# Performance work log

Hardware: AMD Instinct MI355X
Metric: run time of the kernel (lower is better)

The kernel has to match this reference:

```python
import jax, jax.numpy as jnp
import numpy as np

N = 100000      # nodes
E = 1600000     # edges (before self-loops)
F_IN = 128      # dataset.num_node_features
H, C = 8, 8     # heads, hid
D = H * C       # 64, concat output dim
G = 64          # graphs in batch
N_CLS = 10
SLOPE = 0.2     # PyG GATConv negative_slope default


def setup_inputs() -> dict:
    key = jax.random.key(0)
    ks = jax.random.split(key, 16)
    s = 0.1
    return {
        "x": jax.random.normal(ks[0], (N, F_IN), jnp.float32),
        "edge_index": jax.random.randint(ks[1], (2, E), 0, N, jnp.int32),
        "batch": jnp.sort(jax.random.randint(ks[2], (N,), 0, G, jnp.int32)),
        "W1": jax.random.normal(ks[3], (F_IN, D), jnp.float32) * s,
        "a1_src": jax.random.normal(ks[4], (H, C), jnp.float32) * s,
        "a1_dst": jax.random.normal(ks[5], (H, C), jnp.float32) * s,
        "b1": jnp.zeros((D,), jnp.float32),
        "W2": jax.random.normal(ks[6], (D, D), jnp.float32) * s,
        "a2_src": jax.random.normal(ks[7], (H, C), jnp.float32) * s,
        "a2_dst": jax.random.normal(ks[8], (H, C), jnp.float32) * s,
        "b2": jnp.zeros((D,), jnp.float32),
        "W3": jax.random.normal(ks[9], (D, D), jnp.float32) * s,
        "a3_src": jax.random.normal(ks[10], (H, C), jnp.float32) * s,
        "a3_dst": jax.random.normal(ks[11], (H, C), jnp.float32) * s,
        "b3": jnp.zeros((D,), jnp.float32),
        "lin_W": jax.random.normal(ks[12], (D, N_CLS), jnp.float32) * s,
        "lin_b": jnp.zeros((N_CLS,), jnp.float32),
    }


def _gat_conv(h_in, src, dst, W, a_src, a_dst, b):
    # h: [N, H, C] per-head projected features
    h = (h_in @ W).reshape(N, H, C)
    al_src = jnp.einsum('nhc,hc->nh', h, a_src)  # [N, H]
    al_dst = jnp.einsum('nhc,hc->nh', h, a_dst)
    e = al_src[src] + al_dst[dst]                # [E', H]
    e = jnp.where(e > 0, e, SLOPE * e)           # LeakyReLU
    # segment softmax over incoming edges of each dst node
    m = jax.ops.segment_max(e, dst, num_segments=N)          # every node has a self-loop
    e = jnp.exp(e - m[dst])
    denom = jax.ops.segment_sum(e, dst, num_segments=N)
    alpha = e / denom[dst]                        # [E', H]
    out = jax.ops.segment_sum(h[src] * alpha[:, :, None], dst, num_segments=N)
    return out.reshape(N, D) + b


def reference(x, edge_index, batch, W1, a1_src, a1_dst, b1,
              W2, a2_src, a2_dst, b2, W3, a3_src, a3_dst, b3, lin_W, lin_b):
    # PyG GATConv add_self_loops=True
    loop = jnp.arange(N, dtype=edge_index.dtype)
    src = jnp.concatenate([edge_index[0], loop])
    dst = jnp.concatenate([edge_index[1], loop])

    h = jax.nn.elu(_gat_conv(x, src, dst, W1, a1_src, a1_dst, b1))
    h = jax.nn.elu(_gat_conv(h, src, dst, W2, a2_src, a2_dst, b2))
    h = jax.nn.elu(_gat_conv(h, src, dst, W3, a3_src, a3_dst, b3))

    # global mean pool over graph assignment
    sums = jax.ops.segment_sum(h, batch, num_segments=G)          # [G, D]
    cnts = jax.ops.segment_sum(jnp.ones((N,), h.dtype), batch, num_segments=G)
    pooled = sums / jnp.maximum(cnts, 1.0)[:, None]

    return pooled @ lin_W + lin_b  # [G, N_CLS]
```

## Files before the change

### kernel.cpp

```cpp
#include <hip/hip_runtime.h>
#include <math.h>

#define NN 100000
#define EE 1600000
#define GG 64
#define NCLS 10

#define BSH 8
#define NB 391
#define BCAP 4608
#define EPS 4096
#define CAPS 5120

typedef unsigned int uint32;

__device__ __forceinline__ unsigned short f2bf(float f) {
    unsigned u = __float_as_uint(f);
    unsigned r = (u + 0x7fffu + ((u >> 16) & 1u)) >> 16;
    return (unsigned short)r;
}


__global__ __launch_bounds__(512) void bscatter_kernel(
    const int* __restrict__ src, const int* __restrict__ dst,
    int* __restrict__ bfill, uint32* __restrict__ bpack, int n) {
    __shared__ int hist[512], gbase[512], lbase[512], cnt2[512];
    __shared__ int wtot[8];
    __shared__ uint32 lsd[EPS];
    __shared__ unsigned short bkt[EPS];
    int tid = threadIdx.x;
    int lane = tid & 63, wv = tid >> 6;
    int e0 = blockIdx.x * EPS;
    int e1 = min(e0 + EPS, n);

    hist[tid] = 0;
    cnt2[tid] = 0;
    __syncthreads();
    for (int e = e0 + tid; e < e1; e += 512) atomicAdd(&hist[dst[e] >> BSH], 1);
    __syncthreads();
    int h = hist[tid];
    int inc = h;
#pragma unroll
    for (int off = 1; off < 64; off <<= 1) {
        int t = __shfl_up(inc, off);
        if (lane >= off) inc += t;
    }
    if (lane == 63) wtot[wv] = inc;
    __syncthreads();
    if (tid < 8) {
        int t = wtot[tid];
#pragma unroll
        for (int off = 1; off < 8; off <<= 1) {
            int u = __shfl_up(t, off, 8);
            if (tid >= off) t += u;
        }
        wtot[tid] = t;
    }
    __syncthreads();
    if (wv > 0) inc += wtot[wv - 1];
    int lb = inc - h;
    lbase[tid] = lb;
    int go = h > 0 ? atomicAdd(&bfill[tid], h) : 0;
    gbase[tid] = tid * BCAP + go - lb;
    __syncthreads();
    for (int e = e0 + tid; e < e1; e += 512) {
        int s = src[e], dd = dst[e];
        int b = dd >> BSH;
        int r = atomicAdd(&cnt2[b], 1);
        int slot = lbase[b] + r;
        lsd[slot] = ((uint32)s << 8) | (uint32)(dd & 255);
        bkt[slot] = (unsigned short)b;
    }
    __syncthreads();
    int m = e1 - e0;
    for (int i = tid; i < m; i += 512)
        bpack[gbase[bkt[i]] + i] = lsd[i];
}

__global__ __launch_bounds__(256) void bsort_kernel(
    const uint32* __restrict__ bpack, const int* __restrict__ bfill,
    int* __restrict__ rp, int* __restrict__ re, int* __restrict__ col) {
    __shared__ int cnt[256], cnt2[256];
    __shared__ int wtot[4];
    __shared__ int stage[CAPS];
    int b = blockIdx.x;
    int tid = threadIdx.x;
    int ebeg = b * BCAP;
    int sz = bfill[b];
    int n0 = b << BSH;
    int nn = min(256, NN - n0);

    cnt[tid] = 0;
    cnt2[tid] = 0;
    __syncthreads();
    const uint4* bq = (const uint4*)(bpack + ebeg);
    int nq = sz >> 2;
    for (int i = tid; i < nq; i += 256) {
        uint4 p = bq[i];
        atomicAdd(&cnt[p.x & 255u], 1);
        atomicAdd(&cnt[p.y & 255u], 1);
        atomicAdd(&cnt[p.z & 255u], 1);
        atomicAdd(&cnt[p.w & 255u], 1);
    }
    for (int e = (nq << 2) + tid; e < sz; e += 256)
        atomicAdd(&cnt[bpack[ebeg + e] & 255u], 1);
    __syncthreads();
    int lane = tid & 63, wv = tid >> 6;
    int c = cnt[tid];
    int inc = c;
#pragma unroll
    for (int off = 1; off < 64; off <<= 1) {
        int t = __shfl_up(inc, off);
        if (lane >= off) inc += t;
    }
    if (lane == 63) wtot[wv] = inc;
    __syncthreads();
    if (tid < 4) {
        int t = wtot[tid];
#pragma unroll
        for (int off = 1; off < 4; off <<= 1) {
            int u = __shfl_up(t, off, 4);
            if (tid >= off) t += u;
        }
        wtot[tid] = t;
    }
    __syncthreads();
    if (wv > 0) inc += wtot[wv - 1];
    int excl = inc - c;
    cnt[tid] = excl;
    if (tid < nn) {
        rp[n0 + tid] = ebeg + excl;
        re[n0 + tid] = ebeg + inc;
    }
    __syncthreads();
    bool fits = sz <= CAPS;
    for (int i = tid; i < nq; i += 256) {
        uint4 p = bq[i];
        int d0 = (int)(p.x & 255u), d1 = (int)(p.y & 255u);
        int d2 = (int)(p.z & 255u), d3 = (int)(p.w & 255u);
        int p0 = cnt[d0] + atomicAdd(&cnt2[d0], 1);
        int p1 = cnt[d1] + atomicAdd(&cnt2[d1], 1);
        int p2 = cnt[d2] + atomicAdd(&cnt2[d2], 1);
        int p3 = cnt[d3] + atomicAdd(&cnt2[d3], 1);
        if (fits) {
            stage[p0] = (int)(p.x >> 8); stage[p1] = (int)(p.y >> 8);
            stage[p2] = (int)(p.z >> 8); stage[p3] = (int)(p.w >> 8);
        } else {
            col[ebeg + p0] = (int)(p.x >> 8); col[ebeg + p1] = (int)(p.y >> 8);
            col[ebeg + p2] = (int)(p.z >> 8); col[ebeg + p3] = (int)(p.w >> 8);
        }
    }
    for (int e = (nq << 2) + tid; e < sz; e += 256) {
        uint32 p = bpack[ebeg + e];
        int dl = (int)(p & 255u);
        int pos = cnt[dl] + atomicAdd(&cnt2[dl], 1);
        if (fits) stage[pos] = (int)(p >> 8);
        else col[ebeg + pos] = (int)(p >> 8);
    }
    __syncthreads();
    if (fits) {
        uint4* colq = (uint4*)(col + ebeg);
        const uint4* stq = (const uint4*)stage;
        for (int i = tid; i < nq; i += 256) colq[i] = stq[i];
        for (int i = (nq << 2) + tid; i < sz; i += 256) col[ebeg + i] = stage[i];
    }
}


template <int K>
__global__ __launch_bounds__(256) void gemm_al_kernel(
    const float* __restrict__ X, const float* __restrict__ W,
    const float* __restrict__ a_src, const float* __restrict__ a_dst,
    unsigned short* __restrict__ H, float* __restrict__ ALs, float* __restrict__ ALd,
    int nrows) {
    const int KC = 64;
    const int KP = KC + 4;
    __shared__ float Xs[64 * (KC + 4)];
    __shared__ float Ws[K * 64];
    int tid = threadIdx.x;
    int r0 = blockIdx.x * 64;
    int validRows = min(64, nrows - r0);

    {
        const float4* Wg = (const float4*)W;
        float4* Ws4 = (float4*)Ws;
        for (int i = tid; i < K * 16; i += 256) Ws4[i] = Wg[i];
    }

    int cg = tid & 15, rg = tid >> 4;
    int rbase = rg * 4;
    float4 acc0 = make_float4(0.f, 0.f, 0.f, 0.f);
    float4 acc1 = acc0, acc2 = acc0, acc3 = acc0;

    const float4* Xg = (const float4*)X;
    const int QG = K / 4;

    for (int kc = 0; kc < K; kc += KC) {
        __syncthreads();
        for (int i = tid; i < 64 * 16; i += 256) {
            int row = i >> 4, q = i & 15;
            float4 v = (row < validRows)
                ? Xg[(size_t)(r0 + row) * QG + (kc >> 2) + q]
                : make_float4(0.f, 0.f, 0.f, 0.f);
            *(float4*)&Xs[row * KP + q * 4] = v;
        }
        __syncthreads();

#pragma unroll 2
        for (int k = 0; k < KC; k += 4) {
            float4 x0 = *(const float4*)&Xs[(rbase + 0) * KP + k];
            float4 x1 = *(const float4*)&Xs[(rbase + 1) * KP + k];
            float4 x2 = *(const float4*)&Xs[(rbase + 2) * KP + k];
            float4 x3 = *(const float4*)&Xs[(rbase + 3) * KP + k];
            float4 w0 = *(const float4*)&Ws[(kc + k + 0) * 64 + 4 * cg];
            float4 w1 = *(const float4*)&Ws[(kc + k + 1) * 64 + 4 * cg];
            float4 w2 = *(const float4*)&Ws[(kc + k + 2) * 64 + 4 * cg];
            float4 w3 = *(const float4*)&Ws[(kc + k + 3) * 64 + 4 * cg];
#define FMA4(A, S, WV) \
            A.x = fmaf(S, WV.x, A.x); A.y = fmaf(S, WV.y, A.y); \
            A.z = fmaf(S, WV.z, A.z); A.w = fmaf(S, WV.w, A.w)
            FMA4(acc0, x0.x, w0); FMA4(acc1, x1.x, w0); FMA4(acc2, x2.x, w0); FMA4(acc3, x3.x, w0);
            FMA4(acc0, x0.y, w1); FMA4(acc1, x1.y, w1); FMA4(acc2, x2.y, w1); FMA4(acc3, x3.y, w1);
            FMA4(acc0, x0.z, w2); FMA4(acc1, x1.z, w2); FMA4(acc2, x2.z, w2); FMA4(acc3, x3.z, w2);
            FMA4(acc0, x0.w, w3); FMA4(acc1, x1.w, w3); FMA4(acc2, x2.w, w3); FMA4(acc3, x3.w, w3);
#undef FMA4
        }
    }

    int hh = cg >> 1;
    float4 as4 = ((const float4*)a_src)[cg];
    float4 ad4 = ((const float4*)a_dst)[cg];
    float4 accs[4] = {acc0, acc1, acc2, acc3};
#pragma unroll
    for (int i = 0; i < 4; ++i) {
        int r = r0 + rbase + i;
        if (r < nrows) {
            ushort4 p;
            p.x = f2bf(accs[i].x); p.y = f2bf(accs[i].y);
            p.z = f2bf(accs[i].z); p.w = f2bf(accs[i].w);
            ((ushort4*)H)[(size_t)r * 16 + cg] = p;
            float ps = accs[i].x * as4.x + accs[i].y * as4.y +
                       accs[i].z * as4.z + accs[i].w * as4.w;
            float pd = accs[i].x * ad4.x + accs[i].y * ad4.y +
                       accs[i].z * ad4.z + accs[i].w * ad4.w;
            ps += __shfl_xor(ps, 1);
            pd += __shfl_xor(pd, 1);
            if ((cg & 1) == 0) {
                ALs[r * 8 + hh] = ps;
                ALd[r * 8 + hh] = pd;
            }
        }
    }
}


__global__ __launch_bounds__(256, 6) void agg_kernel(
    const unsigned short* __restrict__ H, const float* __restrict__ ALs,
    const float* __restrict__ ALd, const int* __restrict__ rp,
    const int* __restrict__ re, const int* __restrict__ col,
    const float* __restrict__ bias, float* __restrict__ Out, int n) {
    int tid = threadIdx.x;
    int lane = tid & 63;
    int slot = lane >> 3, head = lane & 7;
    int wid = blockIdx.x * 4 + (tid >> 6);
    int d = wid * 8 + slot;
    bool active = d < n;
    if (!active) d = n - 1;
    const uint4* __restrict__ Hq = (const uint4*)H;

    float ad = ALd[d * 8 + head];
    float acc0 = 0.f, acc1 = 0.f, acc2 = 0.f, acc3 = 0.f;
    float acc4 = 0.f, acc5 = 0.f, acc6 = 0.f, acc7 = 0.f;
    float wsum = 0.f;

#define FMA8(U, W) { \
    acc0 = fmaf(W, __uint_as_float((U).x << 16), acc0); \
    acc1 = fmaf(W, __uint_as_float((U).x & 0xffff0000u), acc1); \
    acc2 = fmaf(W, __uint_as_float((U).y << 16), acc2); \
    acc3 = fmaf(W, __uint_as_float((U).y & 0xffff0000u), acc3); \
    acc4 = fmaf(W, __uint_as_float((U).z << 16), acc4); \
    acc5 = fmaf(W, __uint_as_float((U).z & 0xffff0000u), acc5); \
    acc6 = fmaf(W, __uint_as_float((U).w << 16), acc6); \
    acc7 = fmaf(W, __uint_as_float((U).w & 0xffff0000u), acc7); }

    {
        uint4 u = Hq[(size_t)d * 8 + head];
        float e = ALs[d * 8 + head] + ad;
        e = fmaxf(e, 0.2f * e);
        float w = __expf(e);
        FMA8(u, w);
        wsum = w;
    }

    int k = rp[d], kend = re[d];
    for (; k + 4 <= kend; k += 4) {
        int s0 = col[k], s1 = col[k + 1], s2 = col[k + 2], s3 = col[k + 3];
        uint4 u0 = Hq[(size_t)s0 * 8 + head];
        uint4 u1 = Hq[(size_t)s1 * 8 + head];
        uint4 u2 = Hq[(size_t)s2 * 8 + head];
        uint4 u3 = Hq[(size_t)s3 * 8 + head];
        float a0 = ALs[s0 * 8 + head];
        float a1 = ALs[s1 * 8 + head];
        float a2 = ALs[s2 * 8 + head];
        float a3 = ALs[s3 * 8 + head];
        float e0 = a0 + ad; e0 = fmaxf(e0, 0.2f * e0); float w0 = __expf(e0);
        float e1 = a1 + ad; e1 = fmaxf(e1, 0.2f * e1); float w1 = __expf(e1);
        float e2 = a2 + ad; e2 = fmaxf(e2, 0.2f * e2); float w2 = __expf(e2);
        float e3 = a3 + ad; e3 = fmaxf(e3, 0.2f * e3); float w3 = __expf(e3);
        FMA8(u0, w0);
        FMA8(u1, w1);
        FMA8(u2, w2);
        FMA8(u3, w3);
        wsum += (w0 + w1) + (w2 + w3);
    }
    if (k + 2 <= kend) {
        int s0 = col[k], s1 = col[k + 1];
        uint4 u0 = Hq[(size_t)s0 * 8 + head];
        uint4 u1 = Hq[(size_t)s1 * 8 + head];
        float a0 = ALs[s0 * 8 + head];
        float a1 = ALs[s1 * 8 + head];
        float e0 = a0 + ad; e0 = fmaxf(e0, 0.2f * e0); float w0 = __expf(e0);
        float e1 = a1 + ad; e1 = fmaxf(e1, 0.2f * e1); float w1 = __expf(e1);
        FMA8(u0, w0);
        FMA8(u1, w1);
        wsum += w0 + w1;
        k += 2;
    }
    if (k < kend) {
        int s = col[k];
        uint4 u = Hq[(size_t)s * 8 + head];
        float a = ALs[s * 8 + head];
        float e = a + ad; e = fmaxf(e, 0.2f * e);
        float w = __expf(e);
        FMA8(u, w);
        wsum += w;
    }
#undef FMA8

    if (active) {
        float inv = 1.f / wsum;
        float4 b0 = ((const float4*)bias)[head * 2];
        float4 b1 = ((const float4*)bias)[head * 2 + 1];
        float4 o0, o1;
        o0.x = fmaf(acc0, inv, b0.x); o0.x = o0.x > 0.f ? o0.x : expm1f(o0.x);
        o0.y = fmaf(acc1, inv, b0.y); o0.y = o0.y > 0.f ? o0.y : expm1f(o0.y);
        o0.z = fmaf(acc2, inv, b0.z); o0.z = o0.z > 0.f ? o0.z : expm1f(o0.z);
        o0.w = fmaf(acc3, inv, b0.w); o0.w = o0.w > 0.f ? o0.w : expm1f(o0.w);
        o1.x = fmaf(acc4, inv, b1.x); o1.x = o1.x > 0.f ? o1.x : expm1f(o1.x);
        o1.y = fmaf(acc5, inv, b1.y); o1.y = o1.y > 0.f ? o1.y : expm1f(o1.y);
        o1.z = fmaf(acc6, inv, b1.z); o1.z = o1.z > 0.f ? o1.z : expm1f(o1.z);
        o1.w = fmaf(acc7, inv, b1.w); o1.w = o1.w > 0.f ? o1.w : expm1f(o1.w);
        ((float4*)Out)[(size_t)d * 16 + head * 2] = o0;
        ((float4*)Out)[(size_t)d * 16 + head * 2 + 1] = o1;
    }
}


__global__ void pool_kernel(const float* __restrict__ H, const int* __restrict__ batch,
                            float* __restrict__ sums, float* __restrict__ cnt, int n) {
    int gw = (int)((blockIdx.x * blockDim.x + threadIdx.x) >> 6);
    int lane = threadIdx.x & 63;
    int n0 = gw * 64;
    if (n0 >= n) return;
    int n1 = min(n0 + 64, n);
    int curb = batch[n0];
    float local = 0.f, c_local = 0.f;
    for (int i = n0; i < n1; ++i) {
        int b = batch[i];
        if (b != curb) {
            atomicAdd(&sums[curb * 64 + lane], local);
            if (lane == 0) atomicAdd(&cnt[curb], c_local);
            local = 0.f;
            c_local = 0.f;
            curb = b;
        }
        local += H[(size_t)i * 64 + lane];
        c_local += 1.f;
    }
    atomicAdd(&sums[curb * 64 + lane], local);
    if (lane == 0) atomicAdd(&cnt[curb], c_local);
}

__global__ void final_kernel(const float* __restrict__ sums, const float* __restrict__ cnt,
                             const float* __restrict__ W, const float* __restrict__ b,
                             float* __restrict__ out) {
    int t = blockIdx.x * blockDim.x + threadIdx.x;
    if (t >= GG * NCLS) return;
    int g = t / NCLS, k = t % NCLS;
    float c = cnt[g];
    if (c < 1.f) c = 1.f;
    float inv = 1.f / c;
    float acc = b[k];
#pragma unroll
    for (int cc = 0; cc < 64; ++cc)
        acc = fmaf(sums[g * 64 + cc] * inv, W[cc * NCLS + k], acc);
    out[t] = acc;
}


extern "C" void kernel_launch(void* const* d_in, const int* in_sizes, int n_in,
                              void* d_out, int out_size, void* d_ws, size_t ws_size,
                              hipStream_t stream) {
    const float* x    = (const float*)d_in[0];
    const int*   ei   = (const int*)d_in[1];
    const int*   batch = (const int*)d_in[2];
    const float* W1 = (const float*)d_in[3];
    const float* a1s = (const float*)d_in[4];
    const float* a1d = (const float*)d_in[5];
    const float* b1 = (const float*)d_in[6];
    const float* W2 = (const float*)d_in[7];
    const float* a2s = (const float*)d_in[8];
    const float* a2d = (const float*)d_in[9];
    const float* b2 = (const float*)d_in[10];
    const float* W3 = (const float*)d_in[11];
    const float* a3s = (const float*)d_in[12];
    const float* a3d = (const float*)d_in[13];
    const float* b3 = (const float*)d_in[14];
    const float* linW = (const float*)d_in[15];
    const float* linb = (const float*)d_in[16];
    float* out = (float*)d_out;

    char* ws = (char*)d_ws;
    size_t off = 0;
    auto alloc = [&](size_t bytes) -> void* {
        void* p = ws + off;
        off = (off + bytes + 255) & ~(size_t)255;
        return p;
    };
    unsigned short* hBf = (unsigned short*)alloc((size_t)NN * 64 * 2);
    float* hF     = (float*)alloc((size_t)NN * 64 * 4);
    float* ALs    = (float*)alloc((size_t)NN * 8 * 4);
    float* ALd    = (float*)alloc((size_t)NN * 8 * 4);
    int*   rp     = (int*)alloc((size_t)NN * 4);
    int*   reArr  = (int*)alloc((size_t)NN * 4);
    int*   bfill  = (int*)alloc((size_t)NB * 4);
    uint32* bpack = (uint32*)alloc((size_t)NB * BCAP * 4);
    int*   col    = (int*)alloc((size_t)NB * BCAP * 4);
    float* sums   = (float*)alloc((size_t)(GG * 64 + GG) * 4);
    float* gcnt   = sums + GG * 64;

    const int NBLK = (NN + 255) / 256;
    const int SB = (EE + EPS - 1) / EPS;

    hipMemsetAsync(bfill, 0, (size_t)NB * 4, stream);
    bscatter_kernel<<<SB, 512, 0, stream>>>(ei, ei + EE, bfill, bpack, EE);
    bsort_kernel<<<NB, 256, 0, stream>>>(bpack, bfill, rp, reArr, col);

    const int GB = (NN + 63) / 64;
    const int AB = (NN + 31) / 32;

    gemm_al_kernel<128><<<GB, 256, 0, stream>>>(x, W1, a1s, a1d, hBf, ALs, ALd, NN);
    agg_kernel<<<AB, 256, 0, stream>>>(hBf, ALs, ALd, rp, reArr, col, b1, hF, NN);

    gemm_al_kernel<64><<<GB, 256, 0, stream>>>(hF, W2, a2s, a2d, hBf, ALs, ALd, NN);
    agg_kernel<<<AB, 256, 0, stream>>>(hBf, ALs, ALd, rp, reArr, col, b2, hF, NN);

    gemm_al_kernel<64><<<GB, 256, 0, stream>>>(hF, W3, a3s, a3d, hBf, ALs, ALd, NN);
    agg_kernel<<<AB, 256, 0, stream>>>(hBf, ALs, ALd, rp, reArr, col, b3, hF, NN);

    hipMemsetAsync(sums, 0, (size_t)(GG * 64 + GG) * 4, stream);
    pool_kernel<<<NBLK, 256, 0, stream>>>(hF, batch, sums, gcnt, NN);
    final_kernel<<<3, 256, 0, stream>>>(sums, gcnt, linW, linb, out);
}
```

Baseline: 394.7 us.

## Fuse first-layer GEMM with edge bucket scatter in one horizontal launch

Merges the layer-1 projection GEMM and the edge bucket-scatter into one kernel launch. The first 782 blocks compute 128-row GEMM tiles and the remaining blocks do the scatter, sharing LDS through a union. The two independent stages can then overlap on the GPU and one launch is saved. In exchange the GEMM uses a new 128-row, 512-thread tiling with a large LDS footprint, which may lower occupancy for the scatter blocks.

```diff
diff --git a/kernel.cpp b/kernel.cpp
--- a/kernel.cpp
+++ b/kernel.cpp
@@ -11,6 +11,7 @@
 #define BCAP 4608
 #define EPS 4096
 #define CAPS 5120
+#define GB128 782
 
 typedef unsigned int uint32;
 
@@ -21,60 +22,151 @@
 }
 
 
-__global__ __launch_bounds__(512) void bscatter_kernel(
-    const int* __restrict__ src, const int* __restrict__ dst,
-    int* __restrict__ bfill, uint32* __restrict__ bpack, int n) {
-    __shared__ int hist[512], gbase[512], lbase[512], cnt2[512];
-    __shared__ int wtot[8];
-    __shared__ uint32 lsd[EPS];
-    __shared__ unsigned short bkt[EPS];
+union FusedSmem {
+    struct {
+        float Xs[128 * 68];
+        float Ws[128 * 64];
+    } g;
+    struct {
+        int hist[512], gbase[512], lbase[512], cnt2[512];
+        int wtot[8];
+        uint32 lsd[EPS];
+        unsigned short bkt[EPS];
+    } s;
+};
+
+__global__ __launch_bounds__(512) void fused_gemm_bscatter_kernel(
+    const float* __restrict__ X, const float* __restrict__ W,
+    const float* __restrict__ a_src, const float* __restrict__ a_dst,
+    unsigned short* __restrict__ H, float* __restrict__ ALs, float* __restrict__ ALd,
+    int nrows,
+    const int* __restrict__ esrc, const int* __restrict__ edst,
+    int* __restrict__ bfill, uint32* __restrict__ bpack, int nedge) {
+    __shared__ FusedSmem sm;
     int tid = threadIdx.x;
-    int lane = tid & 63, wv = tid >> 6;
-    int e0 = blockIdx.x * EPS;
-    int e1 = min(e0 + EPS, n);
-
-    hist[tid] = 0;
-    cnt2[tid] = 0;
-    __syncthreads();
-    for (int e = e0 + tid; e < e1; e += 512) atomicAdd(&hist[dst[e] >> BSH], 1);
-    __syncthreads();
-    int h = hist[tid];
-    int inc = h;
-#pragma unroll
-    for (int off = 1; off < 64; off <<= 1) {
-        int t = __shfl_up(inc, off);
-        if (lane >= off) inc += t;
-    }
-    if (lane == 63) wtot[wv] = inc;
-    __syncthreads();
-    if (tid < 8) {
-        int t = wtot[tid];
-#pragma unroll
-        for (int off = 1; off < 8; off <<= 1) {
-            int u = __shfl_up(t, off, 8);
-            if (tid >= off) t += u;
-        }
-        wtot[tid] = t;
-    }
-    __syncthreads();
-    if (wv > 0) inc += wtot[wv - 1];
-    int lb = inc - h;
-    lbase[tid] = lb;
-    int go = h > 0 ? atomicAdd(&bfill[tid], h) : 0;
-    gbase[tid] = tid * BCAP + go - lb;
-    __syncthreads();
-    for (int e = e0 + tid; e < e1; e += 512) {
-        int s = src[e], dd = dst[e];
-        int b = dd >> BSH;
-        int r = atomicAdd(&cnt2[b], 1);
-        int slot = lbase[b] + r;
-        lsd[slot] = ((uint32)s << 8) | (uint32)(dd & 255);
-        bkt[slot] = (unsigned short)b;
-    }
-    __syncthreads();
-    int m = e1 - e0;
-    for (int i = tid; i < m; i += 512)
-        bpack[gbase[bkt[i]] + i] = lsd[i];
+
+    if (blockIdx.x < GB128) {
+        const int K = 128, KC = 64, KP = KC + 4, QG = K / 4;
+        int r0 = blockIdx.x * 128;
+        int validRows = min(128, nrows - r0);
+
+        {
+            const float4* Wg = (const float4*)W;
+            float4* Ws4 = (float4*)sm.g.Ws;
+            for (int i = tid; i < K * 16; i += 512) Ws4[i] = Wg[i];
+        }
+
+        int cg = tid & 15, rg = tid >> 4;
+        int rbase = rg * 4;
+        float4 acc0 = make_float4(0.f, 0.f, 0.f, 0.f);
+        float4 acc1 = acc0, acc2 = acc0, acc3 = acc0;
+        const float4* Xg = (const float4*)X;
+
+        for (int kc = 0; kc < K; kc += KC) {
+            __syncthreads();
+            for (int i = tid; i < 128 * 16; i += 512) {
+                int row = i >> 4, q = i & 15;
+                float4 v = (row < validRows)
+                    ? Xg[(size_t)(r0 + row) * QG + (kc >> 2) + q]
+                    : make_float4(0.f, 0.f, 0.f, 0.f);
+                *(float4*)&sm.g.Xs[row * KP + q * 4] = v;
+            }
+            __syncthreads();
+
+#pragma unroll 2
+            for (int k = 0; k < KC; k += 4) {
+                float4 x0 = *(const float4*)&sm.g.Xs[(rbase + 0) * KP + k];
+                float4 x1 = *(const float4*)&sm.g.Xs[(rbase + 1) * KP + k];
+                float4 x2 = *(const float4*)&sm.g.Xs[(rbase + 2) * KP + k];
+                float4 x3 = *(const float4*)&sm.g.Xs[(rbase + 3) * KP + k];
+                float4 w0 = *(const float4*)&sm.g.Ws[(kc + k + 0) * 64 + 4 * cg];
+                float4 w1 = *(const float4*)&sm.g.Ws[(kc + k + 1) * 64 + 4 * cg];
+                float4 w2 = *(const float4*)&sm.g.Ws[(kc + k + 2) * 64 + 4 * cg];
+                float4 w3 = *(const float4*)&sm.g.Ws[(kc + k + 3) * 64 + 4 * cg];
+#define FMA4(A, S, WV) \
+                A.x = fmaf(S, WV.x, A.x); A.y = fmaf(S, WV.y, A.y); \
+                A.z = fmaf(S, WV.z, A.z); A.w = fmaf(S, WV.w, A.w)
+                FMA4(acc0, x0.x, w0); FMA4(acc1, x1.x, w0); FMA4(acc2, x2.x, w0); FMA4(acc3, x3.x, w0);
+                FMA4(acc0, x0.y, w1); FMA4(acc1, x1.y, w1); FMA4(acc2, x2.y, w1); FMA4(acc3, x3.y, w1);
+                FMA4(acc0, x0.z, w2); FMA4(acc1, x1.z, w2); FMA4(acc2, x2.z, w2); FMA4(acc3, x3.z, w2);
+                FMA4(acc0, x0.w, w3); FMA4(acc1, x1.w, w3); FMA4(acc2, x2.w, w3); FMA4(acc3, x3.w, w3);
+#undef FMA4
+            }
+        }
+
+        int hh = cg >> 1;
+        float4 as4 = ((const float4*)a_src)[cg];
+        float4 ad4 = ((const float4*)a_dst)[cg];
+        float4 accs[4] = {acc0, acc1, acc2, acc3};
+#pragma unroll
+        for (int i = 0; i < 4; ++i) {
+            int r = r0 + rbase + i;
+            if (r < nrows) {
+                ushort4 p;
+                p.x = f2bf(accs[i].x); p.y = f2bf(accs[i].y);
+                p.z = f2bf(accs[i].z); p.w = f2bf(accs[i].w);
+                ((ushort4*)H)[(size_t)r * 16 + cg] = p;
+                float ps = accs[i].x * as4.x + accs[i].y * as4.y +
+                           accs[i].z * as4.z + accs[i].w * as4.w;
+                float pd = accs[i].x * ad4.x + accs[i].y * ad4.y +
+                           accs[i].z * ad4.z + accs[i].w * ad4.w;
+                ps += __shfl_xor(ps, 1);
+                pd += __shfl_xor(pd, 1);
+                if ((cg & 1) == 0) {
+                    ALs[r * 8 + hh] = ps;
+                    ALd[r * 8 + hh] = pd;
+                }
+            }
+        }
+    } else {
+        int lane = tid & 63, wv = tid >> 6;
+        int bb = blockIdx.x - GB128;
+        int e0 = bb * EPS;
+        int e1 = min(e0 + EPS, nedge);
+
+        sm.s.hist[tid] = 0;
+        sm.s.cnt2[tid] = 0;
+        __syncthreads();
+        for (int e = e0 + tid; e < e1; e += 512) atomicAdd(&sm.s.hist[edst[e] >> BSH], 1);
+        __syncthreads();
+        int h = sm.s.hist[tid];
+        int inc = h;
+#pragma unroll
+        for (int off = 1; off < 64; off <<= 1) {
+            int t = __shfl_up(inc, off);
+            if (lane >= off) inc += t;
+        }
+        if (lane == 63) sm.s.wtot[wv] = inc;
+        __syncthreads();
+        if (tid < 8) {
+            int t = sm.s.wtot[tid];
+#pragma unroll
+            for (int off = 1; off < 8; off <<= 1) {
+                int u = __shfl_up(t, off, 8);
+                if (tid >= off) t += u;
+            }
+            sm.s.wtot[tid] = t;
+        }
+        __syncthreads();
+        if (wv > 0) inc += sm.s.wtot[wv - 1];
+        int lb = inc - h;
+        sm.s.lbase[tid] = lb;
+        int go = h > 0 ? atomicAdd(&bfill[tid], h) : 0;
+        sm.s.gbase[tid] = tid * BCAP + go - lb;
+        __syncthreads();
+        for (int e = e0 + tid; e < e1; e += 512) {
+            int s = esrc[e], dd = edst[e];
+            int b = dd >> BSH;
+            int r = atomicAdd(&sm.s.cnt2[b], 1);
+            int slot = sm.s.lbase[b] + r;
+            sm.s.lsd[slot] = ((uint32)s << 8) | (uint32)(dd & 255);
+            sm.s.bkt[slot] = (unsigned short)b;
+        }
+        __syncthreads();
+        int m = e1 - e0;
+        for (int i = tid; i < m; i += 512)
+            bpack[sm.s.gbase[sm.s.bkt[i]] + i] = sm.s.lsd[i];
+    }
 }
 
 __global__ __launch_bounds__(256) void bsort_kernel(
@@ -443,13 +535,14 @@
     const int SB = (EE + EPS - 1) / EPS;
 
     hipMemsetAsync(bfill, 0, (size_t)NB * 4, stream);
-    bscatter_kernel<<<SB, 512, 0, stream>>>(ei, ei + EE, bfill, bpack, EE);
+
+    fused_gemm_bscatter_kernel<<<GB128 + SB, 512, 0, stream>>>(
+        x, W1, a1s, a1d, hBf, ALs, ALd, NN, ei, ei + EE, bfill, bpack, EE);
     bsort_kernel<<<NB, 256, 0, stream>>>(bpack, bfill, rp, reArr, col);
 
     const int GB = (NN + 63) / 64;
     const int AB = (NN + 31) / 32;
 
-    gemm_al_kernel<128><<<GB, 256, 0, stream>>>(x, W1, a1s, a1d, hBf, ALs, ALd, NN);
     agg_kernel<<<AB, 256, 0, stream>>>(hBf, ALs, ALd, rp, reArr, col, b1, hF, NN);
 
     gemm_al_kernel<64><<<GB, 256, 0, stream>>>(hF, W2, a2s, a2d, hBf, ALs, ALd, NN);
```

Measured after the change: 402.5 us. About the same (+2.0%).
